# Optimization experiments

Measured on AMD Instinct MI355X. Metric: run time of the kernel, lower is better.

## Reference

```python
import jax, jax.numpy as jnp
import numpy as np

HID = 50

def _lstm_cell(x_t, h, c, W_ih, W_hh, b_ih, b_hh):
    # PyTorch LSTMCell gate order: i, f, g, o
    gates = x_t @ W_ih.T + b_ih + h @ W_hh.T + b_hh  # [B, 4*HID]
    i, f, g, o = jnp.split(gates, 4, axis=-1)
    i = jax.nn.sigmoid(i)
    f = jax.nn.sigmoid(f)
    g = jnp.tanh(g)
    o = jax.nn.sigmoid(o)
    c = f * c + i * g
    h = o * jnp.tanh(c)
    return h, c


def setup_inputs() -> dict:
    key = jax.random.key(0)
    ks = jax.random.split(key, 8)
    B, T = 2048, 512
    stdv = 1.0 / np.sqrt(HID)
    x = jax.random.normal(ks[0], (B, T), dtype=jnp.float32)
    W_ih = jax.random.uniform(ks[1], (4 * HID, 1), jnp.float32, -stdv, stdv)
    W_hh = jax.random.uniform(ks[2], (4 * HID, HID), jnp.float32, -stdv, stdv)
    b_ih = jax.random.uniform(ks[3], (4 * HID,), jnp.float32, -stdv, stdv)
    b_hh = jax.random.uniform(ks[4], (4 * HID,), jnp.float32, -stdv, stdv)
    W_out = jax.random.uniform(ks[5], (1, HID), jnp.float32, -stdv, stdv)
    b_out = jax.random.uniform(ks[6], (1,), jnp.float32, -stdv, stdv)
    return {"x": x, "W_ih": W_ih, "W_hh": W_hh, "b_ih": b_ih,
            "b_hh": b_hh, "W_out": W_out, "b_out": b_out, "future": 64}


def reference(x, W_ih, W_hh, b_ih, b_hh, W_out, b_out, future):
    B, T = x.shape
    h0 = jnp.zeros((B, HID), dtype=x.dtype)
    c0 = jnp.zeros((B, HID), dtype=x.dtype)
    xs = x.T[:, :, None]  # [T, B, 1]

    def seq_step(carry, x_t):
        h, c = carry
        h, c = _lstm_cell(x_t, h, c, W_ih, W_hh, b_ih, b_hh)
        out = h @ W_out.T + b_out  # [B, 1]
        return (h, c), out

    (h, c), outs = jax.lax.scan(seq_step, (h0, c0), xs)  # outs: [T, B, 1]

    def fut_step(carry, _):
        h, c, out = carry
        h, c = _lstm_cell(out, h, c, W_ih, W_hh, b_ih, b_hh)
        out = h @ W_out.T + b_out
        return (h, c, out), out

    _, fut_outs = jax.lax.scan(fut_step, (h, c, outs[-1]), None, length=future)
    all_outs = jnp.concatenate([outs, fut_outs], axis=0)  # [T+future, B, 1]
    return jnp.transpose(all_outs[:, :, 0])  # [B, T+future]
```

## Files before the change

### kernel.cpp

```cpp
#include <hip/hip_runtime.h>

typedef float v2f __attribute__((ext_vector_type(2)));
typedef float v4f __attribute__((ext_vector_type(4)));

#define BATCH 2048
#define TSEQ 512
#define FUT 64
#define TOUT (TSEQ + FUT)
#define HID 50
#define RPB 4


__device__ __forceinline__ float rcp_f(float x) { return __builtin_amdgcn_rcpf(x); }
__device__ __forceinline__ float sigm(float x)  { return rcp_f(1.f + __expf(-x)); }
__device__ __forceinline__ float tanh_f(float x){ return 1.f - 2.f * rcp_f(__expf(2.f * x) + 1.f); }

__device__ __forceinline__ void pkfma(v2f& acc, v2f a, v2f b) {
  asm("v_pk_fma_f32 %0, %1, %2, %0" : "+v"(acc) : "v"(a), "v"(b));
}

__global__ __launch_bounds__(256, 2) void lstm_seq_kernel(
    const float* __restrict__ x,
    const float* __restrict__ W_ih,
    const float* __restrict__ W_hh,
    const float* __restrict__ b_ih,
    const float* __restrict__ b_hh,
    const float* __restrict__ W_out,
    const float* __restrict__ b_out,
    float* __restrict__ out)
{
  __shared__ float sx[RPB][TSEQ];
  __shared__ float sH[RPB][64];

  const int tid  = threadIdx.x;
  const int wv   = tid >> 6;
  const int lane = tid & 63;
  const int row  = blockIdx.x * RPB + wv;

  for (int i = tid; i < RPB * TSEQ; i += 256)
    ((float*)sx)[i] = x[blockIdx.x * RPB * TSEQ + i];
  if (tid < RPB * 64) ((float*)sH)[tid] = 0.f;
  __syncthreads();

  const bool act = (lane < HID);
  const int  kk  = act ? lane : 0;

  v2f wi[25], wf[25], wg[25], wo[25];
  {
    const v2f* r0 = (const v2f*)(W_hh + (0 * HID + kk) * HID);
    const v2f* r1 = (const v2f*)(W_hh + (1 * HID + kk) * HID);
    const v2f* r2 = (const v2f*)(W_hh + (2 * HID + kk) * HID);
    const v2f* r3 = (const v2f*)(W_hh + (3 * HID + kk) * HID);
    #pragma unroll
    for (int j = 0; j < 25; ++j) { wi[j] = r0[j]; wf[j] = r1[j]; wg[j] = r2[j]; wo[j] = r3[j]; }
  }
  float bi = b_ih[0 * HID + kk] + b_hh[0 * HID + kk];
  float bf = b_ih[1 * HID + kk] + b_hh[1 * HID + kk];
  float bg = b_ih[2 * HID + kk] + b_hh[2 * HID + kk];
  float bo = b_ih[3 * HID + kk] + b_hh[3 * HID + kk];
  const float wxi = W_ih[0 * HID + kk];
  const float wxf = W_ih[1 * HID + kk];
  const float wxg = W_ih[2 * HID + kk];
  const float wxo = W_ih[3 * HID + kk];
  const float wout = act ? W_out[kk] : 0.f;
  const float bout = b_out[0];

  float h = 0.f, c = 0.f;
  float* orow = out + (size_t)row * TOUT;
  const v4f* sH4 = (const v4f*)sH[wv];
  const v2f* sH2 = (const v2f*)sH[wv];

  #pragma unroll 1
  for (int t = 0; t < TOUT; ++t) {
    if (t == TSEQ) {
      const v2f* wo2 = (const v2f*)W_out;
      const v2f xi = {wxi, wxi}, xf = {wxf, wxf}, xg = {wxg, wxg}, xo = {wxo, wxo};
      #pragma unroll
      for (int j = 0; j < 25; ++j) {
        const v2f wv_ = wo2[j];
        pkfma(wi[j], xi, wv_);
        pkfma(wf[j], xf, wv_);
        pkfma(wg[j], xg, wv_);
        pkfma(wo[j], xo, wv_);
      }
      bi = fmaf(wxi, bout, bi);
      bf = fmaf(wxf, bout, bf);
      bg = fmaf(wxg, bout, bg);
      bo = fmaf(wxo, bout, bo);
    }
    const float xv = (t < TSEQ) ? sx[wv][t] : 0.f;

    sH[wv][lane] = h;

    v2f ai = {fmaf(xv, wxi, bi), 0.f};
    v2f af = {fmaf(xv, wxf, bf), 0.f};
    v2f ag = {fmaf(xv, wxg, bg), 0.f};
    v2f ao = {fmaf(xv, wxo, bo), 0.f};
    #pragma unroll
    for (int q = 0; q < 12; ++q) {
      const v4f h4 = sH4[q];
      const v2f ha = {h4.x, h4.y}, hb = {h4.z, h4.w};
      pkfma(ai, wi[2 * q], ha); pkfma(ai, wi[2 * q + 1], hb);
      pkfma(af, wf[2 * q], ha); pkfma(af, wf[2 * q + 1], hb);
      pkfma(ag, wg[2 * q], ha); pkfma(ag, wg[2 * q + 1], hb);
      pkfma(ao, wo[2 * q], ha); pkfma(ao, wo[2 * q + 1], hb);
    }
    { const v2f ht = sH2[24];
      pkfma(ai, wi[24], ht); pkfma(af, wf[24], ht);
      pkfma(ag, wg[24], ht); pkfma(ao, wo[24], ht); }

    const float gi = sigm(ai.x + ai.y);
    const float gf = sigm(af.x + af.y);
    const float gg = tanh_f(ag.x + ag.y);
    const float go = sigm(ao.x + ao.y);
    c = fmaf(gf, c, gi * gg);
    h = act ? go * tanh_f(c) : 0.f;

    float p = h * wout;
    p += __shfl_xor(p, 1);
    p += __shfl_xor(p, 2);
    p += __shfl_xor(p, 4);
    p += __shfl_xor(p, 8);
    p += __shfl_xor(p, 16);
    p += __shfl_xor(p, 32);
    if (lane == 0) orow[t] = p + bout;
  }
}

extern "C" void kernel_launch(void* const* d_in, const int* in_sizes, int n_in,
                              void* d_out, int out_size, void* d_ws, size_t ws_size,
                              hipStream_t stream) {
  const float* x     = (const float*)d_in[0];
  const float* W_ih  = (const float*)d_in[1];
  const float* W_hh  = (const float*)d_in[2];
  const float* b_ih  = (const float*)d_in[3];
  const float* b_hh  = (const float*)d_in[4];
  const float* W_out = (const float*)d_in[5];
  const float* b_out = (const float*)d_in[6];
  float* out = (float*)d_out;

  lstm_seq_kernel<<<BATCH / RPB, 256, 0, stream>>>(
      x, W_ih, W_hh, b_ih, b_hh, W_out, b_out, out);
}
```

Before: 584.8 us.

## Process two batch rows per wave to reuse register-resident weights

Each wavefront now advances two independent LSTM rows at once, reusing the register-held W_hh weights for both and interleaving their FMA, activation and shuffle-reduction chains. Block count halves and launch bounds drop to one block per CU, so latency hiding moves from inter-wave occupancy to intra-wave ILP. Risks are higher register pressure and fewer waves per SIMD.

```diff
diff --git a/kernel.cpp b/kernel.cpp
--- a/kernel.cpp
+++ b/kernel.cpp
@@ -8,7 +8,9 @@
 #define FUT 64
 #define TOUT (TSEQ + FUT)
 #define HID 50
-#define RPB 4
+#define RPW 2
+#define WPB 4
+#define RPB (RPW * WPB)
 
 
 __device__ __forceinline__ float rcp_f(float x) { return __builtin_amdgcn_rcpf(x); }
@@ -19,7 +21,7 @@
   asm("v_pk_fma_f32 %0, %1, %2, %0" : "+v"(acc) : "v"(a), "v"(b));
 }
 
-__global__ __launch_bounds__(256, 2) void lstm_seq_kernel(
+__global__ __launch_bounds__(256, 1) void lstm_seq_kernel(
     const float* __restrict__ x,
     const float* __restrict__ W_ih,
     const float* __restrict__ W_hh,
@@ -35,11 +37,11 @@
   const int tid  = threadIdx.x;
   const int wv   = tid >> 6;
   const int lane = tid & 63;
-  const int row  = blockIdx.x * RPB + wv;
+  const int r0   = blockIdx.x * RPB + 2 * wv;
 
   for (int i = tid; i < RPB * TSEQ; i += 256)
-    ((float*)sx)[i] = x[blockIdx.x * RPB * TSEQ + i];
-  if (tid < RPB * 64) ((float*)sH)[tid] = 0.f;
+    ((float*)sx)[i] = x[(size_t)blockIdx.x * RPB * TSEQ + i];
+  for (int i = tid; i < RPB * 64; i += 256) ((float*)sH)[i] = 0.f;
   __syncthreads();
 
   const bool act = (lane < HID);
@@ -47,12 +49,12 @@
 
   v2f wi[25], wf[25], wg[25], wo[25];
   {
-    const v2f* r0 = (const v2f*)(W_hh + (0 * HID + kk) * HID);
-    const v2f* r1 = (const v2f*)(W_hh + (1 * HID + kk) * HID);
-    const v2f* r2 = (const v2f*)(W_hh + (2 * HID + kk) * HID);
-    const v2f* r3 = (const v2f*)(W_hh + (3 * HID + kk) * HID);
+    const v2f* q0 = (const v2f*)(W_hh + (0 * HID + kk) * HID);
+    const v2f* q1 = (const v2f*)(W_hh + (1 * HID + kk) * HID);
+    const v2f* q2 = (const v2f*)(W_hh + (2 * HID + kk) * HID);
+    const v2f* q3 = (const v2f*)(W_hh + (3 * HID + kk) * HID);
     #pragma unroll
-    for (int j = 0; j < 25; ++j) { wi[j] = r0[j]; wf[j] = r1[j]; wg[j] = r2[j]; wo[j] = r3[j]; }
+    for (int j = 0; j < 25; ++j) { wi[j] = q0[j]; wf[j] = q1[j]; wg[j] = q2[j]; wo[j] = q3[j]; }
   }
   float bi = b_ih[0 * HID + kk] + b_hh[0 * HID + kk];
   float bf = b_ih[1 * HID + kk] + b_hh[1 * HID + kk];
@@ -65,10 +67,13 @@
   const float wout = act ? W_out[kk] : 0.f;
   const float bout = b_out[0];
 
-  float h = 0.f, c = 0.f;
-  float* orow = out + (size_t)row * TOUT;
-  const v4f* sH4 = (const v4f*)sH[wv];
-  const v2f* sH2 = (const v2f*)sH[wv];
+  float h0 = 0.f, c0 = 0.f, h1 = 0.f, c1 = 0.f;
+  float* orow0 = out + (size_t)r0 * TOUT;
+  float* orow1 = orow0 + TOUT;
+  const v4f* sH4a = (const v4f*)sH[2 * wv];
+  const v4f* sH4b = (const v4f*)sH[2 * wv + 1];
+  const v2f* sH2a = (const v2f*)sH[2 * wv];
+  const v2f* sH2b = (const v2f*)sH[2 * wv + 1];
 
   #pragma unroll 1
   for (int t = 0; t < TOUT; ++t) {
@@ -88,42 +93,55 @@
       bg = fmaf(wxg, bout, bg);
       bo = fmaf(wxo, bout, bo);
     }
-    const float xv = (t < TSEQ) ? sx[wv][t] : 0.f;
+    const float xv0 = (t < TSEQ) ? sx[2 * wv][t] : 0.f;
+    const float xv1 = (t < TSEQ) ? sx[2 * wv + 1][t] : 0.f;
 
-    sH[wv][lane] = h;
+    sH[2 * wv][lane] = h0;
+    sH[2 * wv + 1][lane] = h1;
 
-    v2f ai = {fmaf(xv, wxi, bi), 0.f};
-    v2f af = {fmaf(xv, wxf, bf), 0.f};
-    v2f ag = {fmaf(xv, wxg, bg), 0.f};
-    v2f ao = {fmaf(xv, wxo, bo), 0.f};
+    v2f ai0 = {fmaf(xv0, wxi, bi), 0.f}, ai1 = {fmaf(xv1, wxi, bi), 0.f};
+    v2f af0 = {fmaf(xv0, wxf, bf), 0.f}, af1 = {fmaf(xv1, wxf, bf), 0.f};
+    v2f ag0 = {fmaf(xv0, wxg, bg), 0.f}, ag1 = {fmaf(xv1, wxg, bg), 0.f};
+    v2f ao0 = {fmaf(xv0, wxo, bo), 0.f}, ao1 = {fmaf(xv1, wxo, bo), 0.f};
     #pragma unroll
     for (int q = 0; q < 12; ++q) {
-      const v4f h4 = sH4[q];
-      const v2f ha = {h4.x, h4.y}, hb = {h4.z, h4.w};
-      pkfma(ai, wi[2 * q], ha); pkfma(ai, wi[2 * q + 1], hb);
-      pkfma(af, wf[2 * q], ha); pkfma(af, wf[2 * q + 1], hb);
-      pkfma(ag, wg[2 * q], ha); pkfma(ag, wg[2 * q + 1], hb);
-      pkfma(ao, wo[2 * q], ha); pkfma(ao, wo[2 * q + 1], hb);
+      const v4f ha4 = sH4a[q];
+      const v4f hb4 = sH4b[q];
+      const v2f haA = {ha4.x, ha4.y}, haB = {ha4.z, ha4.w};
+      const v2f hbA = {hb4.x, hb4.y}, hbB = {hb4.z, hb4.w};
+      pkfma(ai0, wi[2 * q], haA); pkfma(ai0, wi[2 * q + 1], haB);
+      pkfma(ai1, wi[2 * q], hbA); pkfma(ai1, wi[2 * q + 1], hbB);
+      pkfma(af0, wf[2 * q], haA); pkfma(af0, wf[2 * q + 1], haB);
+      pkfma(af1, wf[2 * q], hbA); pkfma(af1, wf[2 * q + 1], hbB);
+      pkfma(ag0, wg[2 * q], haA); pkfma(ag0, wg[2 * q + 1], haB);
+      pkfma(ag1, wg[2 * q], hbA); pkfma(ag1, wg[2 * q + 1], hbB);
+      pkfma(ao0, wo[2 * q], haA); pkfma(ao0, wo[2 * q + 1], haB);
+      pkfma(ao1, wo[2 * q], hbA); pkfma(ao1, wo[2 * q + 1], hbB);
     }
-    { const v2f ht = sH2[24];
-      pkfma(ai, wi[24], ht); pkfma(af, wf[24], ht);
-      pkfma(ag, wg[24], ht); pkfma(ao, wo[24], ht); }
+    { const v2f hta = sH2a[24];
+      const v2f htb = sH2b[24];
+      pkfma(ai0, wi[24], hta); pkfma(ai1, wi[24], htb);
+      pkfma(af0, wf[24], hta); pkfma(af1, wf[24], htb);
+      pkfma(ag0, wg[24], hta); pkfma(ag1, wg[24], htb);
+      pkfma(ao0, wo[24], hta); pkfma(ao1, wo[24], htb); }
 
-    const float gi = sigm(ai.x + ai.y);
-    const float gf = sigm(af.x + af.y);
-    const float gg = tanh_f(ag.x + ag.y);
-    const float go = sigm(ao.x + ao.y);
-    c = fmaf(gf, c, gi * gg);
-    h = act ? go * tanh_f(c) : 0.f;
+    const float gi0 = sigm(ai0.x + ai0.y), gi1 = sigm(ai1.x + ai1.y);
+    const float gf0 = sigm(af0.x + af0.y), gf1 = sigm(af1.x + af1.y);
+    const float gg0 = tanh_f(ag0.x + ag0.y), gg1 = tanh_f(ag1.x + ag1.y);
+    const float go0 = sigm(ao0.x + ao0.y), go1 = sigm(ao1.x + ao1.y);
+    c0 = fmaf(gf0, c0, gi0 * gg0);
+    c1 = fmaf(gf1, c1, gi1 * gg1);
+    h0 = act ? go0 * tanh_f(c0) : 0.f;
+    h1 = act ? go1 * tanh_f(c1) : 0.f;
 
-    float p = h * wout;
-    p += __shfl_xor(p, 1);
-    p += __shfl_xor(p, 2);
-    p += __shfl_xor(p, 4);
-    p += __shfl_xor(p, 8);
-    p += __shfl_xor(p, 16);
-    p += __shfl_xor(p, 32);
-    if (lane == 0) orow[t] = p + bout;
+    float p0 = h0 * wout, p1 = h1 * wout;
+    p0 += __shfl_xor(p0, 1);  p1 += __shfl_xor(p1, 1);
+    p0 += __shfl_xor(p0, 2);  p1 += __shfl_xor(p1, 2);
+    p0 += __shfl_xor(p0, 4);  p1 += __shfl_xor(p1, 4);
+    p0 += __shfl_xor(p0, 8);  p1 += __shfl_xor(p1, 8);
+    p0 += __shfl_xor(p0, 16); p1 += __shfl_xor(p1, 16);
+    p0 += __shfl_xor(p0, 32); p1 += __shfl_xor(p1, 32);
+    if (lane == 0) { orow0[t] = p0 + bout; orow1[t] = p1 + bout; }
   }
 }
 
```

Result: slower. 1.006 ms (+72.0%).
